# Performance work log

Hardware: AMD Instinct MI355X
Metric: run time of the kernel (lower is better)

Reference implementation:

```python
import jax, jax.numpy as jnp
import numpy as np

IN_DIM = 512
OUT_DIM = 512


def setup_inputs() -> dict:
    key = jax.random.key(0)
    ks = jax.random.split(key, 7)
    B, S = 4, 2048
    scale = 1.0 / np.sqrt(IN_DIM)
    X = jax.random.normal(ks[0], (B, S, IN_DIM), dtype=jnp.float32)
    Wq = jax.random.normal(ks[1], (IN_DIM, OUT_DIM), dtype=jnp.float32) * scale
    Wk = jax.random.normal(ks[2], (IN_DIM, OUT_DIM), dtype=jnp.float32) * scale
    Wv = jax.random.normal(ks[3], (IN_DIM, OUT_DIM), dtype=jnp.float32) * scale
    bq = jnp.zeros((OUT_DIM,), dtype=jnp.float32)
    bk = jnp.zeros((OUT_DIM,), dtype=jnp.float32)
    bv = jnp.zeros((OUT_DIM,), dtype=jnp.float32)
    return {"X": X, "Wq": Wq, "bq": bq, "Wk": Wk, "bk": bk, "Wv": Wv, "bv": bv}


def reference(X, Wq, bq, Wk, bk, Wv, bv):
    # Q/K/V projections: [B,S,in] @ [in,out] -> [B,S,out]
    Q = X @ Wq + bq
    K = X @ Wk + bk
    V = X @ Wv + bv
    d_k = jnp.asarray(Q.shape[-1], Q.dtype)
    # scores: [B,S,S] = QK^T / sqrt(d_k)
    scores = jnp.einsum('bsd,btd->bst', Q, K) / jnp.sqrt(d_k)
    attn = jax.nn.softmax(scores, axis=-1)
    # out: [B,S,out]
    return jnp.einsum('bst,btd->bsd', attn, V)
```

## Files before the change

kernel.cpp:

```cpp
#include <hip/hip_runtime.h>
#include <hip/hip_bf16.h>
#include <stdint.h>

#define SEQ   2048
#define DIM   512
#define BATCH 4

typedef __attribute__((ext_vector_type(8))) short  short8;
typedef __attribute__((ext_vector_type(4))) float  floatx4;

static __device__ __forceinline__ unsigned short f2b(float f) {
  return __builtin_bit_cast(unsigned short, __float2bfloat16(f));
}

static __device__ __forceinline__ void gll16(const void* g, void* l) {
  __builtin_amdgcn_global_load_lds(
      (__attribute__((address_space(1))) void*)(uintptr_t)g,
      (__attribute__((address_space(3))) void*)l, 16, 0, 0);
}


template <int AF, int BF, int WM, int WN, int KC>
__device__ __forceinline__ void fgemm8(
    const char* __restrict__ A, int rtA0, int TKA,
    const char* __restrict__ B, int rtB0, int TKB,
    int kIters, char* lds, floatx4 (&acc)[AF / WM][BF / WN])
{
  constexpr int AWF = AF / WM, BWF = BF / WN;
  constexpr int BUF = (AF + BF) * KC * 1024;
  const int tid = threadIdx.x;
  const int w = tid >> 6, l = tid & 63;
  const int wm = w % WM, wn = w / WM;

  auto stage = [&](int p, int kt) {
    char* dst = lds + p * BUF;
#pragma unroll
    for (int c = 0; c < KC; ++c) {
#pragma unroll
      for (int q = 0; q < AF / 8; ++q) {
        const int f = q * 8 + w;
        gll16(A + (((size_t)(rtA0 + f) * TKA + kt * KC + c) << 10) + l * 16,
              dst + (c * AF + f) * 1024 + l * 16);
      }
#pragma unroll
      for (int q = 0; q < BF / 8; ++q) {
        const int f = q * 8 + w;
        gll16(B + (((size_t)(rtB0 + f) * TKB + kt * KC + c) << 10) + l * 16,
              dst + (KC * AF + c * BF + f) * 1024 + l * 16);
      }
    }
  };

  stage(0, 0);
  __syncthreads();

  for (int kt = 0; kt < kIters; ++kt) {
    const int p = kt & 1;
    if (kt + 1 < kIters) stage(1 - p, kt + 1);

    const char* bA = lds + p * BUF;
    const char* bB = bA + KC * AF * 1024;
    short8 af[KC][AWF], bf[KC][BWF];
#pragma unroll
    for (int c = 0; c < KC; ++c) {
#pragma unroll
      for (int i = 0; i < AWF; ++i)
        af[c][i] = *(const short8*)(bA + (c * AF + wm * AWF + i) * 1024 + l * 16);
#pragma unroll
      for (int j = 0; j < BWF; ++j)
        bf[c][j] = *(const short8*)(bB + (c * BF + wn * BWF + j) * 1024 + l * 16);
    }
#pragma unroll
    for (int c = 0; c < KC; ++c)
#pragma unroll
      for (int i = 0; i < AWF; ++i)
#pragma unroll
        for (int j = 0; j < BWF; ++j)
          acc[i][j] = __builtin_amdgcn_mfma_f32_16x16x32_bf16(af[c][i], bf[c][j], acc[i][j], 0, 0, 0);

    __syncthreads();
  }
}

__global__ __launch_bounds__(256) void setup_kernel(
    const float* __restrict__ X, const float* __restrict__ Wq,
    const float* __restrict__ Wk, const float* __restrict__ Wv,
    short8* __restrict__ XbF, short8* __restrict__ WF,
    float* __restrict__ rowsum)
{
  const int flat = blockIdx.x * 256 + threadIdx.x;
  {
    const int tile = flat >> 6, l = flat & 63;
    const int row = (tile >> 4) * 16 + (l & 15);
    const int k0  = (tile & 15) * 32 + (l >> 4) * 8;
    const float4 v0 = *(const float4*)(X + (size_t)row * DIM + k0);
    const float4 v1 = *(const float4*)(X + (size_t)row * DIM + k0 + 4);
    short8 o;
    o[0] = (short)f2b(v0.x); o[1] = (short)f2b(v0.y);
    o[2] = (short)f2b(v0.z); o[3] = (short)f2b(v0.w);
    o[4] = (short)f2b(v1.x); o[5] = (short)f2b(v1.y);
    o[6] = (short)f2b(v1.z); o[7] = (short)f2b(v1.w);
    XbF[flat] = o;
  }
  if (flat < 3 * 32768) {
    const int z = flat >> 15, within = flat & 32767;
    const float* W = (z == 0) ? Wq : (z == 1) ? Wk : Wv;
    const int tile = within >> 6, l = within & 63;
    const int n  = (tile >> 4) * 16 + (l & 15);
    const int k0 = (tile & 15) * 32 + (l >> 4) * 8;
    short8 o;
#pragma unroll
    for (int e = 0; e < 8; ++e)
      o[e] = (short)f2b(W[(size_t)(k0 + e) * DIM + n]);
    WF[flat] = o;
  }
  if (flat < 2048) ((float4*)rowsum)[flat] = float4{0.f, 0.f, 0.f, 0.f};
}

__global__ __launch_bounds__(512, 2) void qkv_kernel(
    const short8* __restrict__ XbF, const short8* __restrict__ WF,
    const float* __restrict__ bq, const float* __restrict__ bk,
    const float* __restrict__ bv,
    unsigned short* __restrict__ QF, unsigned short* __restrict__ KF,
    unsigned short* __restrict__ VF)
{
  __shared__ char lds[49152];
  const int z = blockIdx.z, job = blockIdx.x;
  const int lane = threadIdx.x & 63, w = threadIdx.x >> 6;
  const int wm = w & 3, wn = w >> 2;
  const char* Xc = (const char*)XbF;
  const char* Wc = (const char*)WF;
  floatx4 acc[4][4] = {};

  if (z < 2) {
    const int x = job & 63, y = job >> 6;
    fgemm8<16, 8, 4, 2, 1>(Wc + (size_t)z * 524288, y * 16, 16,
                           Xc, x * 8, 16, 16, lds, acc);
    const float* bias = z ? bk : bq;
    unsigned short* OF = z ? KF : QF;
    const int dbase = y * 256 + wm * 64;
    const int sbase = x * 128 + wn * 64;
#pragma unroll
    for (int i = 0; i < 4; ++i) {
      const int d0 = dbase + i * 16 + (lane >> 4) * 4;
      const float4 b4 = *(const float4*)(bias + d0);
#pragma unroll
      for (int j = 0; j < 4; ++j) {
        const int s = sbase + j * 16 + (lane & 15);
        ushort4 pk;
        pk.x = f2b(acc[i][j][0] + b4.x);
        pk.y = f2b(acc[i][j][1] + b4.y);
        pk.z = f2b(acc[i][j][2] + b4.z);
        pk.w = f2b(acc[i][j][3] + b4.w);
        *(ushort4*)(OF + (size_t)((s >> 4) * 16 + (d0 >> 5)) * 512 +
                    ((((d0 & 31) >> 3) << 4) | (s & 15)) * 8 + (d0 & 7)) = pk;
      }
    }
  } else {
    const int x = job >> 2, y = job & 3;
    fgemm8<16, 8, 4, 2, 1>(Xc, x * 16, 16,
                           Wc + 2 * 524288, y * 8, 16, 16, lds, acc);
    const int sbase = x * 256 + wm * 64;
    const int dbase = y * 128 + wn * 64;
#pragma unroll
    for (int i = 0; i < 4; ++i) {
      const int s0 = sbase + i * 16 + (lane >> 4) * 4;
      const int bt = s0 >> 11, t0 = s0 & 2047;
#pragma unroll
      for (int j = 0; j < 4; ++j) {
        const int d = dbase + j * 16 + (lane & 15);
        const float bn = bv[d];
        ushort4 pk;
        pk.x = f2b(acc[i][j][0] + bn);
        pk.y = f2b(acc[i][j][1] + bn);
        pk.z = f2b(acc[i][j][2] + bn);
        pk.w = f2b(acc[i][j][3] + bn);
        *(ushort4*)(VF + (size_t)bt * DIM * SEQ +
                    (size_t)((d >> 4) * 64 + (t0 >> 5)) * 512 +
                    ((((t0 & 31) >> 3) << 4) | (d & 15)) * 8 + (t0 & 7)) = pk;
      }
    }
  }
}

__global__ __launch_bounds__(512, 2) void scores_kernel(
    const unsigned short* __restrict__ QF, const unsigned short* __restrict__ KF,
    unsigned short* __restrict__ ScF, float* __restrict__ rowsum)
{
  __shared__ char lds[65536];
  const int b = blockIdx.z, x = blockIdx.x, y = blockIdx.y;
  const int lane = threadIdx.x & 63, w = threadIdx.x >> 6;
  const int wm = w & 1, wn = w >> 1;
  floatx4 acc[8][4] = {};
  fgemm8<16, 16, 2, 4, 1>((const char*)KF + (size_t)b * 2097152, y * 16, 16,
                          (const char*)QF + (size_t)b * 2097152, x * 16, 16,
                          16, lds, acc);

  unsigned short* S = ScF + (size_t)b * SEQ * SEQ;
  const float scale = 0.044194173824159216f;
  const int tbase = y * 256 + wm * 128;
  const int sbase = x * 256 + wn * 64;
  float colsum[4] = {0.f, 0.f, 0.f, 0.f};
#pragma unroll
  for (int i = 0; i < 8; ++i) {
    const int t0 = tbase + i * 16 + (lane >> 4) * 4;
#pragma unroll
    for (int j = 0; j < 4; ++j) {
      const int s = sbase + j * 16 + (lane & 15);
      float e0 = __expf(acc[i][j][0] * scale);
      float e1 = __expf(acc[i][j][1] * scale);
      float e2 = __expf(acc[i][j][2] * scale);
      float e3 = __expf(acc[i][j][3] * scale);
      colsum[j] += (e0 + e1) + (e2 + e3);
      ushort4 pk;
      pk.x = f2b(e0); pk.y = f2b(e1); pk.z = f2b(e2); pk.w = f2b(e3);
      *(ushort4*)(S + (size_t)((s >> 4) * 64 + (t0 >> 5)) * 512 +
                  ((((t0 & 31) >> 3) << 4) | (s & 15)) * 8 + (t0 & 7)) = pk;
    }
  }
#pragma unroll
  for (int j = 0; j < 4; ++j) {
    colsum[j] += __shfl_xor(colsum[j], 16, 64);
    colsum[j] += __shfl_xor(colsum[j], 32, 64);
  }
  if (lane < 16) {
#pragma unroll
    for (int j = 0; j < 4; ++j)
      atomicAdd(rowsum + b * SEQ + sbase + j * 16 + lane, colsum[j]);
  }
}

__global__ __launch_bounds__(512, 2) void pv_kernel(
    const unsigned short* __restrict__ ScF, const unsigned short* __restrict__ VF,
    const float* __restrict__ rowsum, float* __restrict__ out)
{
  __shared__ char lds[65536];
  const int b = blockIdx.z, x = blockIdx.x, y = blockIdx.y;
  const int lane = threadIdx.x & 63, w = threadIdx.x >> 6;
  const int wm = w & 1, wn = w >> 1;
  floatx4 acc[4][2] = {};
  fgemm8<8, 8, 2, 4, 2>((const char*)ScF + (size_t)b * 8388608, x * 8, 64,
                        (const char*)VF + (size_t)b * 2097152, y * 8, 64,
                        32, lds, acc);

  const int mbase = x * 128 + wm * 64;
  const int dbase = y * 128 + wn * 32;
#pragma unroll
  for (int i = 0; i < 4; ++i) {
    const int m0 = mbase + i * 16 + (lane >> 4) * 4;
    const float4 rs = *(const float4*)(rowsum + b * SEQ + m0);
    const float inv0 = 1.f / rs.x, inv1 = 1.f / rs.y, inv2 = 1.f / rs.z, inv3 = 1.f / rs.w;
#pragma unroll
    for (int j = 0; j < 2; ++j) {
      const int d = dbase + j * 16 + (lane & 15);
      float* o = out + ((size_t)b * SEQ + m0) * DIM + d;
      o[0 * DIM] = acc[i][j][0] * inv0;
      o[1 * DIM] = acc[i][j][1] * inv1;
      o[2 * DIM] = acc[i][j][2] * inv2;
      o[3 * DIM] = acc[i][j][3] * inv3;
    }
  }
}

extern "C" void kernel_launch(void* const* d_in, const int* in_sizes, int n_in,
                              void* d_out, int out_size, void* d_ws, size_t ws_size,
                              hipStream_t stream) {
  const float* X  = (const float*)d_in[0];
  const float* Wq = (const float*)d_in[1];
  const float* bq = (const float*)d_in[2];
  const float* Wk = (const float*)d_in[3];
  const float* bk = (const float*)d_in[4];
  const float* Wv = (const float*)d_in[5];
  const float* bv = (const float*)d_in[6];
  float* out = (float*)d_out;
  char* ws = (char*)d_ws;

  short8* XbF = (short8*)(ws + 0);
  short8* WF  = (short8*)(ws + 8388608);
  char*   QF  = ws + 9961472;
  char*   KF  = ws + 18350080;
  char*   VF  = ws + 26738688;
  char*   ScF = ws + 35127296;
  float*  rowsum = (float*)(ws + 68681728);

  setup_kernel<<<dim3(2048), 256, 0, stream>>>(X, Wq, Wk, Wv, XbF, WF, rowsum);
  qkv_kernel<<<dim3(128, 1, 3), 512, 0, stream>>>(
      XbF, WF, bq, bk, bv,
      (unsigned short*)QF, (unsigned short*)KF, (unsigned short*)VF);
  scores_kernel<<<dim3(8, 8, 4), 512, 0, stream>>>(
      (const unsigned short*)QF, (const unsigned short*)KF,
      (unsigned short*)ScF, rowsum);
  pv_kernel<<<dim3(16, 4, 4), 512, 0, stream>>>(
      (const unsigned short*)ScF, (const unsigned short*)VF, rowsum, out);
}
```

Before: 150.4 us.

## Use 4-slot LDS pipeline with 3-deep prefetch and larger QKV tiles

Replaces the double-buffered GEMM core with a four-slot LDS ring that prefetches three K-steps ahead. Each step waits on explicit vmcnt counts plus a barrier instead of a full __syncthreads. MFMA sections run at raised wave priority via s_setprio. QKV blocks grow to 256x256 tiles with half the grid, reusing more data per block. The cost is 128KB of LDS per block, which likely cuts occupancy to one block per CU despite launch_bounds(512,2), and fewer QKV blocks than CUs.

Result: faster. 146.5 us (-2.5%).

```diff
diff --git a/kernel.cpp b/kernel.cpp
--- a/kernel.cpp
+++ b/kernel.cpp
@@ -20,20 +20,22 @@
 }
 
 
-template <int AF, int BF, int WM, int WN, int KC>
-__device__ __forceinline__ void fgemm8(
+template <int AF, int BF, int WM, int WN, int KC, int KIT>
+__device__ __forceinline__ void fgemm_pipe(
     const char* __restrict__ A, int rtA0, int TKA,
     const char* __restrict__ B, int rtB0, int TKB,
-    int kIters, char* lds, floatx4 (&acc)[AF / WM][BF / WN])
-{
-  constexpr int AWF = AF / WM, BWF = BF / WN;
-  constexpr int BUF = (AF + BF) * KC * 1024;
+    char* lds, floatx4 (&acc)[AF / WM][BF / WN])
+{
+  constexpr int AWF  = AF / WM, BWF = BF / WN;
+  constexpr int SLOT = (AF + BF) * KC * 1024;
+  constexpr int L    = KC * (AF / 8 + BF / 8);
+  static_assert(KIT >= 3, "pipeline needs >=3 K-steps");
   const int tid = threadIdx.x;
   const int w = tid >> 6, l = tid & 63;
   const int wm = w % WM, wn = w / WM;
 
-  auto stage = [&](int p, int kt) {
-    char* dst = lds + p * BUF;
+  auto stage = [&](int slot, int kt) {
+    char* dst = lds + slot * SLOT;
 #pragma unroll
     for (int c = 0; c < KC; ++c) {
 #pragma unroll
@@ -51,14 +53,15 @@
     }
   };
 
-  stage(0, 0);
-  __syncthreads();
-
-  for (int kt = 0; kt < kIters; ++kt) {
-    const int p = kt & 1;
-    if (kt + 1 < kIters) stage(1 - p, kt + 1);
-
-    const char* bA = lds + p * BUF;
+  stage(0, 0); stage(1, 1); stage(2, 2);
+  asm volatile("s_waitcnt vmcnt(%0) lgkmcnt(0)\ns_barrier" :: "n"(2 * L) : "memory");
+
+#pragma unroll 4
+  for (int kt = 0; kt < KIT; ++kt) {
+    const int cslot = kt & 3;
+    if (kt + 3 < KIT) stage((kt + 3) & 3, kt + 3);
+
+    const char* bA = lds + cslot * SLOT;
     const char* bB = bA + KC * AF * 1024;
     short8 af[KC][AWF], bf[KC][BWF];
 #pragma unroll
@@ -70,6 +73,7 @@
       for (int j = 0; j < BWF; ++j)
         bf[c][j] = *(const short8*)(bB + (c * BF + wn * BWF + j) * 1024 + l * 16);
     }
+    __builtin_amdgcn_s_setprio(1);
 #pragma unroll
     for (int c = 0; c < KC; ++c)
 #pragma unroll
@@ -77,8 +81,16 @@
 #pragma unroll
         for (int j = 0; j < BWF; ++j)
           acc[i][j] = __builtin_amdgcn_mfma_f32_16x16x32_bf16(af[c][i], bf[c][j], acc[i][j], 0, 0, 0);
-
-    __syncthreads();
+    __builtin_amdgcn_s_setprio(0);
+
+    if (kt + 1 < KIT) {
+      if (kt + 3 < KIT)
+        asm volatile("s_waitcnt vmcnt(%0) lgkmcnt(0)\ns_barrier" :: "n"(2 * L) : "memory");
+      else if (kt + 2 < KIT)
+        asm volatile("s_waitcnt vmcnt(%0) lgkmcnt(0)\ns_barrier" :: "n"(L) : "memory");
+      else
+        asm volatile("s_waitcnt vmcnt(0) lgkmcnt(0)\ns_barrier" ::: "memory");
+    }
   }
 }
 
@@ -124,24 +136,24 @@
     unsigned short* __restrict__ QF, unsigned short* __restrict__ KF,
     unsigned short* __restrict__ VF)
 {
-  __shared__ char lds[49152];
+  __shared__ char lds[131072];
   const int z = blockIdx.z, job = blockIdx.x;
   const int lane = threadIdx.x & 63, w = threadIdx.x >> 6;
-  const int wm = w & 3, wn = w >> 2;
+  const int wm = w & 1, wn = w >> 1;
+  const int x = job & 31, y = job >> 5;
   const char* Xc = (const char*)XbF;
   const char* Wc = (const char*)WF;
-  floatx4 acc[4][4] = {};
+  floatx4 acc[8][4] = {};
 
   if (z < 2) {
-    const int x = job & 63, y = job >> 6;
-    fgemm8<16, 8, 4, 2, 1>(Wc + (size_t)z * 524288, y * 16, 16,
-                           Xc, x * 8, 16, 16, lds, acc);
+    fgemm_pipe<16, 16, 2, 4, 1, 16>(Wc + (size_t)z * 524288, y * 16, 16,
+                                    Xc, x * 16, 16, lds, acc);
     const float* bias = z ? bk : bq;
     unsigned short* OF = z ? KF : QF;
-    const int dbase = y * 256 + wm * 64;
-    const int sbase = x * 128 + wn * 64;
-#pragma unroll
-    for (int i = 0; i < 4; ++i) {
+    const int dbase = y * 256 + wm * 128;
+    const int sbase = x * 256 + wn * 64;
+#pragma unroll
+    for (int i = 0; i < 8; ++i) {
       const int d0 = dbase + i * 16 + (lane >> 4) * 4;
       const float4 b4 = *(const float4*)(bias + d0);
 #pragma unroll
@@ -157,13 +169,12 @@
       }
     }
   } else {
-    const int x = job >> 2, y = job & 3;
-    fgemm8<16, 8, 4, 2, 1>(Xc, x * 16, 16,
-                           Wc + 2 * 524288, y * 8, 16, 16, lds, acc);
-    const int sbase = x * 256 + wm * 64;
-    const int dbase = y * 128 + wn * 64;
-#pragma unroll
-    for (int i = 0; i < 4; ++i) {
+    fgemm_pipe<16, 16, 2, 4, 1, 16>(Xc, x * 16, 16,
+                                    Wc + 2 * 524288, y * 16, 16, lds, acc);
+    const int sbase = x * 256 + wm * 128;
+    const int dbase = y * 256 + wn * 64;
+#pragma unroll
+    for (int i = 0; i < 8; ++i) {
       const int s0 = sbase + i * 16 + (lane >> 4) * 4;
       const int bt = s0 >> 11, t0 = s0 & 2047;
 #pragma unroll
@@ -187,14 +198,14 @@
     const unsigned short* __restrict__ QF, const unsigned short* __restrict__ KF,
     unsigned short* __restrict__ ScF, float* __restrict__ rowsum)
 {
-  __shared__ char lds[65536];
+  __shared__ char lds[131072];
   const int b = blockIdx.z, x = blockIdx.x, y = blockIdx.y;
   const int lane = threadIdx.x & 63, w = threadIdx.x >> 6;
   const int wm = w & 1, wn = w >> 1;
   floatx4 acc[8][4] = {};
-  fgemm8<16, 16, 2, 4, 1>((const char*)KF + (size_t)b * 2097152, y * 16, 16,
-                          (const char*)QF + (size_t)b * 2097152, x * 16, 16,
-                          16, lds, acc);
+  fgemm_pipe<16, 16, 2, 4, 1, 16>((const char*)KF + (size_t)b * 2097152, y * 16, 16,
+                                  (const char*)QF + (size_t)b * 2097152, x * 16, 16,
+                                  lds, acc);
 
   unsigned short* S = ScF + (size_t)b * SEQ * SEQ;
   const float scale = 0.044194173824159216f;
@@ -234,14 +245,14 @@
     const unsigned short* __restrict__ ScF, const unsigned short* __restrict__ VF,
     const float* __restrict__ rowsum, float* __restrict__ out)
 {
-  __shared__ char lds[65536];
+  __shared__ char lds[131072];
   const int b = blockIdx.z, x = blockIdx.x, y = blockIdx.y;
   const int lane = threadIdx.x & 63, w = threadIdx.x >> 6;
   const int wm = w & 1, wn = w >> 1;
   floatx4 acc[4][2] = {};
-  fgemm8<8, 8, 2, 4, 2>((const char*)ScF + (size_t)b * 8388608, x * 8, 64,
-                        (const char*)VF + (size_t)b * 2097152, y * 8, 64,
-                        32, lds, acc);
+  fgemm_pipe<8, 8, 2, 4, 2, 32>((const char*)ScF + (size_t)b * 8388608, x * 8, 64,
+                                (const char*)VF + (size_t)b * 2097152, y * 8, 64,
+                                lds, acc);
 
   const int mbase = x * 128 + wm * 64;
   const int dbase = y * 128 + wn * 32;
@@ -284,7 +295,7 @@
   float*  rowsum = (float*)(ws + 68681728);
 
   setup_kernel<<<dim3(2048), 256, 0, stream>>>(X, Wq, Wk, Wv, XbF, WF, rowsum);
-  qkv_kernel<<<dim3(128, 1, 3), 512, 0, stream>>>(
+  qkv_kernel<<<dim3(64, 1, 3), 512, 0, stream>>>(
       XbF, WF, bq, bk, bv,
       (unsigned short*)QF, (unsigned short*)KF, (unsigned short*)VF);
   scores_kernel<<<dim3(8, 8, 4), 512, 0, stream>>>(
```
